# Optimization experiments

Hardware: AMD Instinct MI355X
Metric: run time of the kernel (lower is better)

## Reference

```python
import jax, jax.numpy as jnp
import numpy as np

TREE_DEPTH = 6
IN_F, OUT_F = 1024, 1024
BATCH = 2048
N_LEAVES = 2 ** TREE_DEPTH
N_NODES = N_LEAVES - 1


def _tree_routes(depth):
    """Static routing table: for each leaf, the decision-node index visited at
    each depth and whether the leaf takes the sigmoid (1) or 1-sigmoid (0) branch.
    Mirrors the torch traversal: node = 2*node + 1 + bit; bits of leaf id LSB-first."""
    n_leaves = 2 ** depth
    idx = np.zeros((n_leaves, depth), dtype=np.int32)
    pos = np.zeros((n_leaves, depth), dtype=bool)
    for l in range(n_leaves):
        node, index = 0, l
        for d in range(depth):
            idx[l, d] = node
            pos[l, d] = (index % 2 == 0)
            node = node * 2 + 1 + index % 2
            index >>= 1
    return idx, pos

ROUTE_IDX, ROUTE_POS = _tree_routes(TREE_DEPTH)


def setup_inputs() -> dict:
    key = jax.random.key(0)
    kx, kwd, kwl = jax.random.split(key, 3)
    scale = 0.02  # keep sigmoid/softmax logits in a sane range
    x = jax.random.normal(kx, (BATCH, IN_F), dtype=jnp.float32)
    Wd = jax.random.normal(kwd, (N_NODES, IN_F), dtype=jnp.float32) * scale
    bd = jnp.zeros((N_NODES,), dtype=jnp.float32)
    Wl = jax.random.normal(kwl, (N_LEAVES, OUT_F, IN_F), dtype=jnp.float32) * scale
    bl = jnp.zeros((N_LEAVES, OUT_F), dtype=jnp.float32)
    return {"x": x, "Wd": Wd, "bd": bd, "Wl": Wl, "bl": bl}


def reference(x, Wd, bd, Wl, bl):
    # All decision node probabilities in one GEMM: [B, n_nodes]
    dprob = jax.nn.sigmoid(x @ Wd.T + bd)
    # Gather per-leaf path probs [B, L, depth] and take path product -> routing [B, L]
    path = dprob[:, ROUTE_IDX]                      # [B, L, D]
    path = jnp.where(ROUTE_POS, path, 1.0 - path)
    routing = jnp.prod(path, axis=-1)               # [B, L]
    # All leaf experts in one batched GEMM: [B, L, out], softmax over out (torch dim=1)
    leaf_logits = jnp.einsum('bi,loi->blo', x, Wl) + bl
    leaves = jax.nn.softmax(leaf_logits, axis=-1)
    # Routing-weighted sum over leaves
    return jnp.einsum('bl,blo->bo', routing, leaves)
```

## Files before the change

kernel.cpp:

```cpp
#include <hip/hip_runtime.h>
#include <hip/hip_bf16.h>

#define BATCH 2048
#define KD 1024
#define ND 1024
#define NLEAF 64
#define BM 256
#define BN 256
#define BKT 32
#define NKT (KD / BKT)

typedef __attribute__((ext_vector_type(8))) short bf16x8;
typedef __attribute__((ext_vector_type(4))) float f32x4;
typedef __attribute__((ext_vector_type(4))) _Float16 f16x4;

#define WLB_OFF 0ULL
#define XB_OFF  134217728ULL
#define RT_OFF  138412032ULL
#define LG_OFF  138936320ULL

__device__ __forceinline__ unsigned short f2bf(float f) {
  unsigned int u = __float_as_uint(f);
  u += 0x7fffu + ((u >> 16) & 1u);
  return (unsigned short)(u >> 16);
}

__device__ __forceinline__ void gload_lds16(const void* g, void* l) {
  __builtin_amdgcn_global_load_lds(
      (const __attribute__((address_space(1))) unsigned int*)g,
      (__attribute__((address_space(3))) unsigned int*)l, 16, 0, 0);
}

__global__ void __launch_bounds__(256) convert_kernel(
    const float* __restrict__ Wl, const float* __restrict__ x,
    unsigned short* __restrict__ wlb, unsigned short* __restrict__ xb) {
  const long long WL4 = 16777216LL;
  const long long X4  = 524288LL;
  long long i = (long long)blockIdx.x * 256 + threadIdx.x;
  const long long stride = (long long)gridDim.x * 256;
  for (; i < WL4 + X4; i += stride) {
    float4 v;
    if (i < WL4) v = ((const float4*)Wl)[i];
    else         v = ((const float4*)x)[i - WL4];
    ushort4 o;
    o.x = f2bf(v.x); o.y = f2bf(v.y); o.z = f2bf(v.z); o.w = f2bf(v.w);
    if (i < WL4) ((ushort4*)wlb)[i] = o;
    else         ((ushort4*)xb)[i - WL4] = o;
  }
}

__global__ void __launch_bounds__(256) routing_kernel(
    const float* __restrict__ x, const float* __restrict__ Wd,
    const float* __restrict__ bd, float* __restrict__ rt) {
  __shared__ float xs[4][KD];
  __shared__ float sdp[4][64];
  const int tid = threadIdx.x;
  const int b0 = blockIdx.x * 4;
  const float4* xsrc = (const float4*)(x + (size_t)b0 * KD);
  float4* xdst = (float4*)&xs[0][0];
  for (int i = tid; i < KD; i += 256) xdst[i] = xsrc[i];
  __syncthreads();
  const int wv = tid >> 6, ln = tid & 63;
  const int b = b0 + wv;
  if (ln < 63) {
    const float4* wrow = (const float4*)(Wd + (size_t)ln * KD);
    const float4* xr = (const float4*)&xs[wv][0];
    float4 a = {0.f, 0.f, 0.f, 0.f};
    for (int k = 0; k < KD / 4; ++k) {
      float4 w = wrow[k], xv = xr[k];
      a.x += w.x * xv.x; a.y += w.y * xv.y; a.z += w.z * xv.z; a.w += w.w * xv.w;
    }
    float z = a.x + a.y + a.z + a.w + bd[ln];
    sdp[wv][ln] = 1.f / (1.f + __expf(-z));
  }
  __syncthreads();
  float prod = 1.f;
  int node = 0, index = ln;
  for (int d = 0; d < 6; ++d) {
    float pv = sdp[wv][node];
    prod *= (index & 1) ? (1.f - pv) : pv;
    node = node * 2 + 1 + (index & 1);
    index >>= 1;
  }
  rt[(size_t)b * NLEAF + ln] = prod;
}

__global__ void __launch_bounds__(512, 2) gemm_kernel(
    const unsigned short* __restrict__ A, const unsigned short* __restrict__ B,
    _Float16* __restrict__ C, int ntile) {
  extern __shared__ char smem[];
  const int tid = threadIdx.x;
  const int w = tid >> 6, ln = tid & 63;
  const int wm = w >> 2, wn = w & 3;
  const int g = ln >> 4, r16 = ln & 15;
  const int bid = blockIdx.x;
  const int j = bid >> 3;
  const int bm = (j & 7) * BM;
  const int bn = (((j >> 3) << 3) + (bid & 7)) * BN;
  const long long ldc = (long long)ntile * 256;

  const int rS = tid >> 2;
  const int cS = tid & 3;
  const int csrc = cS ^ ((rS >> 1) & 3);
  const unsigned short* ga0 = A + (size_t)(bm + rS) * KD + csrc * 8;
  const unsigned short* ga1 = ga0 + (size_t)128 * KD;
  const unsigned short* gb0 = B + (size_t)(bn + rS) * KD + csrc * 8;
  const unsigned short* gb1 = gb0 + (size_t)128 * KD;
  const int ldsw = w * 1024;

  auto STAGE_A = [&](int tile) {
    char* base = smem + (tile & 3) * 32768;
    const size_t ko = (size_t)tile * BKT;
    gload_lds16(ga0 + ko, base + ldsw);
    gload_lds16(ga1 + ko, base + 8192 + ldsw);
  };
  auto STAGE_B = [&](int tile) {
    char* base = smem + (tile & 3) * 32768;
    const size_t ko = (size_t)tile * BKT;
    gload_lds16(gb0 + ko, base + 16384 + ldsw);
    gload_lds16(gb1 + ko, base + 24576 + ldsw);
  };

  int offA[8], offB[4];
#pragma unroll
  for (int mi = 0; mi < 8; ++mi) {
    const int row = wm * 128 + mi * 16 + r16;
    offA[mi] = row * 64 + (g ^ ((row >> 1) & 3)) * 16;
  }
#pragma unroll
  for (int ni = 0; ni < 4; ++ni) {
    const int row = wn * 64 + ni * 16 + r16;
    offB[ni] = 16384 + row * 64 + (g ^ ((row >> 1) & 3)) * 16;
  }

  f32x4 acc[8][4];
#pragma unroll
  for (int mi = 0; mi < 8; ++mi)
#pragma unroll
    for (int ni = 0; ni < 4; ++ni) acc[mi][ni] = (f32x4){0.f, 0.f, 0.f, 0.f};

  STAGE_A(0); STAGE_B(0);
  STAGE_A(1); STAGE_B(1);
  STAGE_A(2); STAGE_B(2);
  asm volatile("s_waitcnt vmcnt(8)" ::: "memory");
  asm volatile("s_barrier" ::: "memory");

  for (int t = 0; t < NKT; ++t) {
    const char* buf = smem + (t & 3) * 32768;
    bf16x8 af[4], bfr[4];
#pragma unroll
    for (int ni = 0; ni < 4; ++ni) bfr[ni] = *(const bf16x8*)(buf + offB[ni]);
#pragma unroll
    for (int mi = 0; mi < 4; ++mi) af[mi] = *(const bf16x8*)(buf + offA[mi]);
    if (t + 3 < NKT) STAGE_A(t + 3);
    asm volatile("s_barrier" ::: "memory");
    asm volatile("s_waitcnt lgkmcnt(0)" ::: "memory");
    __builtin_amdgcn_sched_barrier(0);
    __builtin_amdgcn_s_setprio(1);
#pragma unroll
    for (int mi = 0; mi < 4; ++mi)
#pragma unroll
      for (int ni = 0; ni < 4; ++ni)
        acc[mi][ni] = __builtin_amdgcn_mfma_f32_16x16x32_bf16(
            af[mi], bfr[ni], acc[mi][ni], 0, 0, 0);
    __builtin_amdgcn_s_setprio(0);
    __builtin_amdgcn_sched_barrier(0);
#pragma unroll
    for (int mi = 0; mi < 4; ++mi) af[mi] = *(const bf16x8*)(buf + offA[mi + 4]);
    if (t + 3 < NKT) STAGE_B(t + 3);
    asm volatile("s_barrier" ::: "memory");
    asm volatile("s_waitcnt lgkmcnt(0)" ::: "memory");
    __builtin_amdgcn_sched_barrier(0);
    __builtin_amdgcn_s_setprio(1);
#pragma unroll
    for (int mi = 0; mi < 4; ++mi)
#pragma unroll
      for (int ni = 0; ni < 4; ++ni)
        acc[mi + 4][ni] = __builtin_amdgcn_mfma_f32_16x16x32_bf16(
            af[mi], bfr[ni], acc[mi + 4][ni], 0, 0, 0);
    __builtin_amdgcn_s_setprio(0);
    __builtin_amdgcn_sched_barrier(0);
    if (t + 3 < NKT) {
      asm volatile("s_waitcnt vmcnt(8)" ::: "memory");
    } else if (t + 2 < NKT) {
      asm volatile("s_waitcnt vmcnt(4)" ::: "memory");
    } else if (t + 1 < NKT) {
      asm volatile("s_waitcnt vmcnt(0)" ::: "memory");
    }
    if (t + 1 < NKT) asm volatile("s_barrier" ::: "memory");
  }

#pragma unroll
  for (int mi = 0; mi < 8; ++mi)
#pragma unroll
    for (int q = 0; q < 4; ++q) {
      const long long grow = bm + wm * 128 + mi * 16 + g * 4 + q;
#pragma unroll
      for (int ni = 0; ni < 4; ++ni) {
        const int gcol = bn + wn * 64 + ni * 16 + r16;
        C[grow * ldc + gcol] = (_Float16)acc[mi][ni][q];
      }
    }
}

__global__ void __launch_bounds__(256) smax_kernel(
    const _Float16* __restrict__ Cg, const float* __restrict__ rt,
    const float* __restrict__ bl, float* __restrict__ out,
    int lpg, int l0, int first) {
  __shared__ float reds[2][2][4];
  __shared__ float rts[64];
  const int tid = threadIdx.x;
  const int b = blockIdx.x;
  const int w = tid >> 6, ln = tid & 63;
  const int c0 = tid * 4;
  if (tid < lpg) rts[tid] = rt[(size_t)b * NLEAF + l0 + tid];
  __syncthreads();
  float oacc[4] = {0.f, 0.f, 0.f, 0.f};
  const long long ldc = (long long)lpg * ND;

  for (int jj = 0; jj < lpg; jj += 2) {
    const int par = (jj >> 1) & 1;
    const f16x4 h0 = *(const f16x4*)(Cg + (size_t)b * ldc + jj * ND + c0);
    const f16x4 h1 = *(const f16x4*)(Cg + (size_t)b * ldc + (jj + 1) * ND + c0);
    const float4 bv0 = *(const float4*)(bl + (size_t)(l0 + jj) * ND + c0);
    const float4 bv1 = *(const float4*)(bl + (size_t)(l0 + jj + 1) * ND + c0);
    float e0[4], e1[4], s0 = 0.f, s1 = 0.f;
    e0[0] = __expf((float)h0[0] + bv0.x); e0[1] = __expf((float)h0[1] + bv0.y);
    e0[2] = __expf((float)h0[2] + bv0.z); e0[3] = __expf((float)h0[3] + bv0.w);
    e1[0] = __expf((float)h1[0] + bv1.x); e1[1] = __expf((float)h1[1] + bv1.y);
    e1[2] = __expf((float)h1[2] + bv1.z); e1[3] = __expf((float)h1[3] + bv1.w);
#pragma unroll
    for (int k = 0; k < 4; ++k) { s0 += e0[k]; s1 += e1[k]; }
#pragma unroll
    for (int off = 1; off < 64; off <<= 1) {
      s0 += __shfl_xor(s0, off);
      s1 += __shfl_xor(s1, off);
    }
    if (ln == 0) { reds[par][0][w] = s0; reds[par][1][w] = s1; }
    __syncthreads();
    const float S0 = reds[par][0][0] + reds[par][0][1] + reds[par][0][2] + reds[par][0][3];
    const float S1 = reds[par][1][0] + reds[par][1][1] + reds[par][1][2] + reds[par][1][3];
    const float c0f = rts[jj] / S0;
    const float c1f = rts[jj + 1] / S1;
#pragma unroll
    for (int k = 0; k < 4; ++k) oacc[k] += c0f * e0[k] + c1f * e1[k];
  }

  float* orow = out + (size_t)b * ND + c0;
  if (first) {
    *(float4*)orow = (float4){oacc[0], oacc[1], oacc[2], oacc[3]};
  } else {
    float4 p = *(const float4*)orow;
    p.x += oacc[0]; p.y += oacc[1]; p.z += oacc[2]; p.w += oacc[3];
    *(float4*)orow = p;
  }
}

extern "C" void kernel_launch(void* const* d_in, const int* in_sizes, int n_in,
                              void* d_out, int out_size, void* d_ws, size_t ws_size,
                              hipStream_t stream) {
  const float* x  = (const float*)d_in[0];
  const float* Wd = (const float*)d_in[1];
  const float* bd = (const float*)d_in[2];
  const float* Wl = (const float*)d_in[3];
  const float* bl = (const float*)d_in[4];
  float* out = (float*)d_out;
  char* ws = (char*)d_ws;
  unsigned short* wlb = (unsigned short*)(ws + WLB_OFF);
  unsigned short* xb  = (unsigned short*)(ws + XB_OFF);
  float* rt           = (float*)(ws + RT_OFF);
  _Float16* lg        = (_Float16*)(ws + LG_OFF);

  convert_kernel<<<2048, 256, 0, stream>>>(Wl, x, wlb, xb);
  routing_kernel<<<BATCH / 4, 256, 0, stream>>>(x, Wd, bd, rt);
  hipFuncSetAttribute((const void*)gemm_kernel,
                      hipFuncAttributeMaxDynamicSharedMemorySize, 131072);

  const int ngrp = (ws_size >= LG_OFF + (size_t)BATCH * NLEAF * ND * 2) ? 1 : 4;
  const int lpg = NLEAF / ngrp;
  const int ntile = lpg * (ND / BN);
  for (int grp = 0; grp < ngrp; ++grp) {
    gemm_kernel<<<8 * ntile, 512, 131072, stream>>>(
        xb, wlb + (size_t)grp * lpg * ND * KD, lg, ntile);
    smax_kernel<<<BATCH, 256, 0, stream>>>(lg, rt, bl, out,
                                           lpg, grp * lpg, grp == 0);
  }
}
```

Baseline: 507.3 us.

## Switch GEMM mainloop to BK=64 double-buffered tiles with split-half staging

The leaf GEMM mainloop moves from a 4-stage ring of BK=32 tiles to a 2-stage double buffer of BK=64 tiles. Each tile is split into four 16KB regions (A and B, each in two K-halves), and these are prefetched one region at a time between MFMA phases. The aim is to halve the loop iteration count and the per-tile wait/barrier overhead. The cost is extra s_barriers per iteration and a shallower prefetch distance of one tile, which may expose more global-load latency.

```diff
diff --git a/kernel.cpp b/kernel.cpp
--- a/kernel.cpp
+++ b/kernel.cpp
@@ -7,8 +7,8 @@
 #define NLEAF 64
 #define BM 256
 #define BN 256
-#define BKT 32
-#define NKT (KD / BKT)
+#define BKT 64
+#define NT (KD / BKT)
 
 typedef __attribute__((ext_vector_type(8))) short bf16x8;
 typedef __attribute__((ext_vector_type(4))) float f32x4;
@@ -108,29 +108,25 @@
   const unsigned short* gb1 = gb0 + (size_t)128 * KD;
   const int ldsw = w * 1024;
 
-  auto STAGE_A = [&](int tile) {
-    char* base = smem + (tile & 3) * 32768;
-    const size_t ko = (size_t)tile * BKT;
-    gload_lds16(ga0 + ko, base + ldsw);
-    gload_lds16(ga1 + ko, base + 8192 + ldsw);
-  };
-  auto STAGE_B = [&](int tile) {
-    char* base = smem + (tile & 3) * 32768;
-    const size_t ko = (size_t)tile * BKT;
-    gload_lds16(gb0 + ko, base + 16384 + ldsw);
-    gload_lds16(gb1 + ko, base + 24576 + ldsw);
+  auto STAGE_H = [&](int tile, int region) {
+    char* base = smem + (tile & 1) * 65536 + region * 16384;
+    const unsigned short* g0 = (region >= 2) ? gb0 : ga0;
+    const unsigned short* g1 = (region >= 2) ? gb1 : ga1;
+    const size_t ko = (size_t)tile * BKT + (region & 1) * 32;
+    gload_lds16(g0 + ko, base + ldsw);
+    gload_lds16(g1 + ko, base + 8192 + ldsw);
   };
 
   int offA[8], offB[4];
 #pragma unroll
   for (int mi = 0; mi < 8; ++mi) {
     const int row = wm * 128 + mi * 16 + r16;
-    offA[mi] = row * 64 + (g ^ ((row >> 1) & 3)) * 16;
+    offA[mi] = row * 64 + ((g ^ ((row >> 1) & 3)) * 16);
   }
 #pragma unroll
   for (int ni = 0; ni < 4; ++ni) {
     const int row = wn * 64 + ni * 16 + r16;
-    offB[ni] = 16384 + row * 64 + (g ^ ((row >> 1) & 3)) * 16;
+    offB[ni] = row * 64 + ((g ^ ((row >> 1) & 3)) * 16);
   }
 
   f32x4 acc[8][4];
@@ -139,20 +135,22 @@
 #pragma unroll
     for (int ni = 0; ni < 4; ++ni) acc[mi][ni] = (f32x4){0.f, 0.f, 0.f, 0.f};
 
-  STAGE_A(0); STAGE_B(0);
-  STAGE_A(1); STAGE_B(1);
-  STAGE_A(2); STAGE_B(2);
-  asm volatile("s_waitcnt vmcnt(8)" ::: "memory");
+  STAGE_H(0, 0); STAGE_H(0, 2); STAGE_H(0, 1); STAGE_H(0, 3);
+  asm volatile("s_waitcnt vmcnt(4)" ::: "memory");
   asm volatile("s_barrier" ::: "memory");
 
-  for (int t = 0; t < NKT; ++t) {
-    const char* buf = smem + (t & 3) * 32768;
+  for (int t = 0; t < NT; ++t) {
+    const bool pf = (t + 1 < NT);
+    const char* bufp = smem + (t & 1) * 65536;
     bf16x8 af[4], bfr[4];
-#pragma unroll
-    for (int ni = 0; ni < 4; ++ni) bfr[ni] = *(const bf16x8*)(buf + offB[ni]);
-#pragma unroll
-    for (int mi = 0; mi < 4; ++mi) af[mi] = *(const bf16x8*)(buf + offA[mi]);
-    if (t + 3 < NKT) STAGE_A(t + 3);
+
+#pragma unroll
+    for (int ni = 0; ni < 4; ++ni)
+      bfr[ni] = *(const bf16x8*)(bufp + 32768 + offB[ni]);
+#pragma unroll
+    for (int mi = 0; mi < 4; ++mi)
+      af[mi] = *(const bf16x8*)(bufp + offA[mi]);
+    if (pf) STAGE_H(t + 1, 0);
     asm volatile("s_barrier" ::: "memory");
     asm volatile("s_waitcnt lgkmcnt(0)" ::: "memory");
     __builtin_amdgcn_sched_barrier(0);
@@ -165,9 +163,12 @@
             af[mi], bfr[ni], acc[mi][ni], 0, 0, 0);
     __builtin_amdgcn_s_setprio(0);
     __builtin_amdgcn_sched_barrier(0);
-#pragma unroll
-    for (int mi = 0; mi < 4; ++mi) af[mi] = *(const bf16x8*)(buf + offA[mi + 4]);
-    if (t + 3 < NKT) STAGE_B(t + 3);
+    asm volatile("s_barrier" ::: "memory");
+
+#pragma unroll
+    for (int mi = 0; mi < 4; ++mi)
+      af[mi] = *(const bf16x8*)(bufp + offA[mi + 4]);
+    if (pf) STAGE_H(t + 1, 2);
     asm volatile("s_barrier" ::: "memory");
     asm volatile("s_waitcnt lgkmcnt(0)" ::: "memory");
     __builtin_amdgcn_sched_barrier(0);
@@ -180,14 +181,51 @@
             af[mi], bfr[ni], acc[mi + 4][ni], 0, 0, 0);
     __builtin_amdgcn_s_setprio(0);
     __builtin_amdgcn_sched_barrier(0);
-    if (t + 3 < NKT) {
-      asm volatile("s_waitcnt vmcnt(8)" ::: "memory");
-    } else if (t + 2 < NKT) {
+    if (pf) asm volatile("s_waitcnt vmcnt(4)" ::: "memory");
+    else    asm volatile("s_waitcnt vmcnt(0)" ::: "memory");
+    asm volatile("s_barrier" ::: "memory");
+
+#pragma unroll
+    for (int ni = 0; ni < 4; ++ni)
+      bfr[ni] = *(const bf16x8*)(bufp + 49152 + offB[ni]);
+#pragma unroll
+    for (int mi = 0; mi < 4; ++mi)
+      af[mi] = *(const bf16x8*)(bufp + 16384 + offA[mi]);
+    if (pf) STAGE_H(t + 1, 1);
+    asm volatile("s_barrier" ::: "memory");
+    asm volatile("s_waitcnt lgkmcnt(0)" ::: "memory");
+    __builtin_amdgcn_sched_barrier(0);
+    __builtin_amdgcn_s_setprio(1);
+#pragma unroll
+    for (int mi = 0; mi < 4; ++mi)
+#pragma unroll
+      for (int ni = 0; ni < 4; ++ni)
+        acc[mi][ni] = __builtin_amdgcn_mfma_f32_16x16x32_bf16(
+            af[mi], bfr[ni], acc[mi][ni], 0, 0, 0);
+    __builtin_amdgcn_s_setprio(0);
+    __builtin_amdgcn_sched_barrier(0);
+    asm volatile("s_barrier" ::: "memory");
+
+#pragma unroll
+    for (int mi = 0; mi < 4; ++mi)
+      af[mi] = *(const bf16x8*)(bufp + 16384 + offA[mi + 4]);
+    if (pf) STAGE_H(t + 1, 3);
+    asm volatile("s_barrier" ::: "memory");
+    asm volatile("s_waitcnt lgkmcnt(0)" ::: "memory");
+    __builtin_amdgcn_sched_barrier(0);
+    __builtin_amdgcn_s_setprio(1);
+#pragma unroll
+    for (int mi = 0; mi < 4; ++mi)
+#pragma unroll
+      for (int ni = 0; ni < 4; ++ni)
+        acc[mi + 4][ni] = __builtin_amdgcn_mfma_f32_16x16x32_bf16(
+            af[mi], bfr[ni], acc[mi + 4][ni], 0, 0, 0);
+    __builtin_amdgcn_s_setprio(0);
+    __builtin_amdgcn_sched_barrier(0);
+    if (pf) {
       asm volatile("s_waitcnt vmcnt(4)" ::: "memory");
-    } else if (t + 1 < NKT) {
-      asm volatile("s_waitcnt vmcnt(0)" ::: "memory");
+      asm volatile("s_barrier" ::: "memory");
     }
-    if (t + 1 < NKT) asm volatile("s_barrier" ::: "memory");
   }
 
 #pragma unroll
```

Result: no change. 499.8 us (-1.5%).

## Pre-pack x into MFMA fragment layout and load A operand directly to registers

Applied to the files above, without the earlier changes.

The convert kernel now writes the bf16 copy of x in a fragment-packed layout, so each lane of the GEMM can load its A operand straight from global memory into registers, skipping LDS. Only B is staged through LDS, which halves shared memory per block to 64 KB, and A fragments are double-buffered in registers across k-steps with a simpler one-barrier-per-step pipeline. This removes LDS traffic and barriers for A. In exchange it increases register pressure and sends A reads through global memory and cache on every k-step.

```diff
diff --git a/kernel.cpp b/kernel.cpp
--- a/kernel.cpp
+++ b/kernel.cpp
@@ -7,15 +7,13 @@
 #define NLEAF 64
 #define BM 256
 #define BN 256
-#define BKT 32
-#define NKT (KD / BKT)
 
 typedef __attribute__((ext_vector_type(8))) short bf16x8;
 typedef __attribute__((ext_vector_type(4))) float f32x4;
 typedef __attribute__((ext_vector_type(4))) _Float16 f16x4;
 
 #define WLB_OFF 0ULL
-#define XB_OFF  134217728ULL
+#define XP_OFF  134217728ULL
 #define RT_OFF  138412032ULL
 #define LG_OFF  138936320ULL
 
@@ -33,19 +31,28 @@
 
 __global__ void __launch_bounds__(256) convert_kernel(
     const float* __restrict__ Wl, const float* __restrict__ x,
-    unsigned short* __restrict__ wlb, unsigned short* __restrict__ xb) {
+    unsigned short* __restrict__ wlb, unsigned short* __restrict__ xp) {
   const long long WL4 = 16777216LL;
-  const long long X4  = 524288LL;
+  const long long XJ  = 524288LL;
   long long i = (long long)blockIdx.x * 256 + threadIdx.x;
   const long long stride = (long long)gridDim.x * 256;
-  for (; i < WL4 + X4; i += stride) {
-    float4 v;
-    if (i < WL4) v = ((const float4*)Wl)[i];
-    else         v = ((const float4*)x)[i - WL4];
-    ushort4 o;
-    o.x = f2bf(v.x); o.y = f2bf(v.y); o.z = f2bf(v.z); o.w = f2bf(v.w);
-    if (i < WL4) ((ushort4*)wlb)[i] = o;
-    else         ((ushort4*)xb)[i - WL4] = o;
+  for (; i < WL4 + XJ; i += stride) {
+    if (i < WL4) {
+      float4 v = ((const float4*)Wl)[i];
+      ushort4 o;
+      o.x = f2bf(v.x); o.y = f2bf(v.y); o.z = f2bf(v.z); o.w = f2bf(v.w);
+      ((ushort4*)wlb)[i] = o;
+    } else {
+      const long long jj = i - WL4;
+      const int pt = (int)(jj >> 1), half = (int)(jj & 1);
+      const int f = pt >> 6, l = pt & 63;
+      const int row = (f & 127) * 16 + (l & 15);
+      const int k0 = (f >> 7) * 32 + (l >> 4) * 8 + half * 4;
+      float4 v = *(const float4*)(x + (size_t)row * KD + k0);
+      ushort4 o;
+      o.x = f2bf(v.x); o.y = f2bf(v.y); o.z = f2bf(v.z); o.w = f2bf(v.w);
+      *(ushort4*)(xp + (size_t)f * 512 + l * 8 + half * 4) = o;
+    }
   }
 }
 
@@ -85,8 +92,34 @@
   rt[(size_t)b * NLEAF + ln] = prod;
 }
 
+#define GBODY(CUR, NXT, S, VMASM, LAST)                                     \
+  {                                                                          \
+    if (!(LAST)) {                                                           \
+      _Pragma("unroll")                                                      \
+      for (int mi = 0; mi < 8; ++mi)                                         \
+        NXT[mi] = *(const bf16x8*)(apL +                                     \
+            ((size_t)((S) + 1) * 128 + rf0 + mi) * 512);                     \
+    }                                                                        \
+    if ((S) + 2 < 32) STAGE_B((S) + 2);                                      \
+    asm volatile(VMASM ::: "memory");                                        \
+    asm volatile("s_barrier" ::: "memory");                                  \
+    const char* bbuf = smem + ((S) & 3) * 16384;                             \
+    bf16x8 bfr[4];                                                           \
+    _Pragma("unroll")                                                        \
+    for (int ni = 0; ni < 4; ++ni)                                           \
+      bfr[ni] = *(const bf16x8*)(bbuf + offB[ni]);                           \
+    __builtin_amdgcn_s_setprio(1);                                           \
+    _Pragma("unroll")                                                        \
+    for (int mi = 0; mi < 8; ++mi)                                           \
+      _Pragma("unroll")                                                      \
+      for (int ni = 0; ni < 4; ++ni)                                         \
+        acc[mi][ni] = __builtin_amdgcn_mfma_f32_16x16x32_bf16(               \
+            CUR[mi], bfr[ni], acc[mi][ni], 0, 0, 0);                         \
+    __builtin_amdgcn_s_setprio(0);                                           \
+  }
+
 __global__ void __launch_bounds__(512, 2) gemm_kernel(
-    const unsigned short* __restrict__ A, const unsigned short* __restrict__ B,
+    const unsigned short* __restrict__ Ap, const unsigned short* __restrict__ B,
     _Float16* __restrict__ C, int ntile) {
   extern __shared__ char smem[];
   const int tid = threadIdx.x;
@@ -102,36 +135,26 @@
   const int rS = tid >> 2;
   const int cS = tid & 3;
   const int csrc = cS ^ ((rS >> 1) & 3);
-  const unsigned short* ga0 = A + (size_t)(bm + rS) * KD + csrc * 8;
-  const unsigned short* ga1 = ga0 + (size_t)128 * KD;
   const unsigned short* gb0 = B + (size_t)(bn + rS) * KD + csrc * 8;
   const unsigned short* gb1 = gb0 + (size_t)128 * KD;
   const int ldsw = w * 1024;
 
-  auto STAGE_A = [&](int tile) {
-    char* base = smem + (tile & 3) * 32768;
-    const size_t ko = (size_t)tile * BKT;
-    gload_lds16(ga0 + ko, base + ldsw);
-    gload_lds16(ga1 + ko, base + 8192 + ldsw);
+  auto STAGE_B = [&](int s) {
+    char* base = smem + (s & 3) * 16384;
+    const size_t ko = (size_t)s * 32;
+    gload_lds16(gb0 + ko, base + ldsw);
+    gload_lds16(gb1 + ko, base + 8192 + ldsw);
   };
-  auto STAGE_B = [&](int tile) {
-    char* base = smem + (tile & 3) * 32768;
-    const size_t ko = (size_t)tile * BKT;
-    gload_lds16(gb0 + ko, base + 16384 + ldsw);
-    gload_lds16(gb1 + ko, base + 24576 + ldsw);
-  };
-
-  int offA[8], offB[4];
-#pragma unroll
-  for (int mi = 0; mi < 8; ++mi) {
-    const int row = wm * 128 + mi * 16 + r16;
-    offA[mi] = row * 64 + (g ^ ((row >> 1) & 3)) * 16;
-  }
+
+  int offB[4];
 #pragma unroll
   for (int ni = 0; ni < 4; ++ni) {
     const int row = wn * 64 + ni * 16 + r16;
-    offB[ni] = 16384 + row * 64 + (g ^ ((row >> 1) & 3)) * 16;
-  }
+    offB[ni] = row * 64 + (g ^ ((row >> 1) & 3)) * 16;
+  }
+
+  const int rf0 = (bm >> 4) + wm * 8;
+  const unsigned short* apL = Ap + (size_t)ln * 8;
 
   f32x4 acc[8][4];
 #pragma unroll
@@ -139,56 +162,19 @@
 #pragma unroll
     for (int ni = 0; ni < 4; ++ni) acc[mi][ni] = (f32x4){0.f, 0.f, 0.f, 0.f};
 
-  STAGE_A(0); STAGE_B(0);
-  STAGE_A(1); STAGE_B(1);
-  STAGE_A(2); STAGE_B(2);
-  asm volatile("s_waitcnt vmcnt(8)" ::: "memory");
-  asm volatile("s_barrier" ::: "memory");
-
-  for (int t = 0; t < NKT; ++t) {
-    const char* buf = smem + (t & 3) * 32768;
-    bf16x8 af[4], bfr[4];
-#pragma unroll
-    for (int ni = 0; ni < 4; ++ni) bfr[ni] = *(const bf16x8*)(buf + offB[ni]);
-#pragma unroll
-    for (int mi = 0; mi < 4; ++mi) af[mi] = *(const bf16x8*)(buf + offA[mi]);
-    if (t + 3 < NKT) STAGE_A(t + 3);
-    asm volatile("s_barrier" ::: "memory");
-    asm volatile("s_waitcnt lgkmcnt(0)" ::: "memory");
-    __builtin_amdgcn_sched_barrier(0);
-    __builtin_amdgcn_s_setprio(1);
-#pragma unroll
-    for (int mi = 0; mi < 4; ++mi)
-#pragma unroll
-      for (int ni = 0; ni < 4; ++ni)
-        acc[mi][ni] = __builtin_amdgcn_mfma_f32_16x16x32_bf16(
-            af[mi], bfr[ni], acc[mi][ni], 0, 0, 0);
-    __builtin_amdgcn_s_setprio(0);
-    __builtin_amdgcn_sched_barrier(0);
-#pragma unroll
-    for (int mi = 0; mi < 4; ++mi) af[mi] = *(const bf16x8*)(buf + offA[mi + 4]);
-    if (t + 3 < NKT) STAGE_B(t + 3);
-    asm volatile("s_barrier" ::: "memory");
-    asm volatile("s_waitcnt lgkmcnt(0)" ::: "memory");
-    __builtin_amdgcn_sched_barrier(0);
-    __builtin_amdgcn_s_setprio(1);
-#pragma unroll
-    for (int mi = 0; mi < 4; ++mi)
-#pragma unroll
-      for (int ni = 0; ni < 4; ++ni)
-        acc[mi + 4][ni] = __builtin_amdgcn_mfma_f32_16x16x32_bf16(
-            af[mi], bfr[ni], acc[mi + 4][ni], 0, 0, 0);
-    __builtin_amdgcn_s_setprio(0);
-    __builtin_amdgcn_sched_barrier(0);
-    if (t + 3 < NKT) {
-      asm volatile("s_waitcnt vmcnt(8)" ::: "memory");
-    } else if (t + 2 < NKT) {
-      asm volatile("s_waitcnt vmcnt(4)" ::: "memory");
-    } else if (t + 1 < NKT) {
-      asm volatile("s_waitcnt vmcnt(0)" ::: "memory");
-    }
-    if (t + 1 < NKT) asm volatile("s_barrier" ::: "memory");
-  }
+  bf16x8 aE[8], aO[8];
+  STAGE_B(0);
+#pragma unroll
+  for (int mi = 0; mi < 8; ++mi)
+    aE[mi] = *(const bf16x8*)(apL + ((size_t)rf0 + mi) * 512);
+  STAGE_B(1);
+
+  for (int u = 0; u < 15; ++u) {
+    GBODY(aE, aO, 2 * u,     "s_waitcnt vmcnt(10)", false);
+    GBODY(aO, aE, 2 * u + 1, "s_waitcnt vmcnt(10)", false);
+  }
+  GBODY(aE, aO, 30, "s_waitcnt vmcnt(8)", false);
+  GBODY(aO, aE, 31, "s_waitcnt vmcnt(0)", true);
 
 #pragma unroll
   for (int mi = 0; mi < 8; ++mi)
@@ -267,21 +253,21 @@
   float* out = (float*)d_out;
   char* ws = (char*)d_ws;
   unsigned short* wlb = (unsigned short*)(ws + WLB_OFF);
-  unsigned short* xb  = (unsigned short*)(ws + XB_OFF);
+  unsigned short* xp  = (unsigned short*)(ws + XP_OFF);
   float* rt           = (float*)(ws + RT_OFF);
   _Float16* lg        = (_Float16*)(ws + LG_OFF);
 
-  convert_kernel<<<2048, 256, 0, stream>>>(Wl, x, wlb, xb);
+  convert_kernel<<<2048, 256, 0, stream>>>(Wl, x, wlb, xp);
   routing_kernel<<<BATCH / 4, 256, 0, stream>>>(x, Wd, bd, rt);
   hipFuncSetAttribute((const void*)gemm_kernel,
-                      hipFuncAttributeMaxDynamicSharedMemorySize, 131072);
+                      hipFuncAttributeMaxDynamicSharedMemorySize, 65536);
 
   const int ngrp = (ws_size >= LG_OFF + (size_t)BATCH * NLEAF * ND * 2) ? 1 : 4;
   const int lpg = NLEAF / ngrp;
   const int ntile = lpg * (ND / BN);
   for (int grp = 0; grp < ngrp; ++grp) {
-    gemm_kernel<<<8 * ntile, 512, 131072, stream>>>(
-        xb, wlb + (size_t)grp * lpg * ND * KD, lg, ntile);
+    gemm_kernel<<<8 * ntile, 512, 65536, stream>>>(
+        xp, wlb + (size_t)grp * lpg * ND * KD, lg, ntile);
     smax_kernel<<<BATCH, 256, 0, stream>>>(lg, rt, bl, out,
                                            lpg, grp * lpg, grp == 0);
   }
```

Measured after the change: 554.0 us. +9.2%, slower.

## Double-buffer LDS fragments in registers to overlap reads with MFMA

Applied to the files above, without the earlier changes.

Restructures the GEMM main loop so each iteration issues the full 32 MFMAs on register fragments loaded in the previous step, while the LDS reads for the next k-tile are issued ahead. A and B global-to-LDS staging for a tile is merged into one call, and the two half-iteration barriers become one per tile. The aim is to hide LDS read latency and cut barrier count. The cost is twice the fragment registers, which could pressure occupancy under the 512x2 launch bounds.

```diff
diff --git a/kernel.cpp b/kernel.cpp
--- a/kernel.cpp
+++ b/kernel.cpp
@@ -7,8 +7,6 @@
 #define NLEAF 64
 #define BM 256
 #define BN 256
-#define BKT 32
-#define NKT (KD / BKT)
 
 typedef __attribute__((ext_vector_type(8))) short bf16x8;
 typedef __attribute__((ext_vector_type(4))) float f32x4;
@@ -85,6 +83,33 @@
   rt[(size_t)b * NLEAF + ln] = prod;
 }
 
+#define GBODY(CURA, CURB, NXTA, NXTB, S, VMASM, DOREAD)                      \
+  {                                                                          \
+    if ((S) + 3 < 32) STAGE((S) + 3);                                        \
+    asm volatile(VMASM ::: "memory");                                        \
+    asm volatile("s_waitcnt lgkmcnt(0)" ::: "memory");                       \
+    asm volatile("s_barrier" ::: "memory");                                  \
+    if (DOREAD) {                                                            \
+      const char* nbuf = smem + (((S) + 1) & 3) * 32768;                     \
+      _Pragma("unroll")                                                      \
+      for (int mi = 0; mi < 8; ++mi)                                         \
+        NXTA[mi] = *(const bf16x8*)(nbuf + offA[mi]);                        \
+      _Pragma("unroll")                                                      \
+      for (int ni = 0; ni < 4; ++ni)                                         \
+        NXTB[ni] = *(const bf16x8*)(nbuf + 16384 + offB[ni]);                \
+    }                                                                        \
+    __builtin_amdgcn_sched_barrier(0);                                       \
+    __builtin_amdgcn_s_setprio(1);                                           \
+    _Pragma("unroll")                                                        \
+    for (int mi = 0; mi < 8; ++mi)                                           \
+      _Pragma("unroll")                                                      \
+      for (int ni = 0; ni < 4; ++ni)                                         \
+        acc[mi][ni] = __builtin_amdgcn_mfma_f32_16x16x32_bf16(               \
+            CURA[mi], CURB[ni], acc[mi][ni], 0, 0, 0);                       \
+    __builtin_amdgcn_s_setprio(0);                                           \
+    __builtin_amdgcn_sched_barrier(0);                                       \
+  }
+
 __global__ void __launch_bounds__(512, 2) gemm_kernel(
     const unsigned short* __restrict__ A, const unsigned short* __restrict__ B,
     _Float16* __restrict__ C, int ntile) {
@@ -108,15 +133,11 @@
   const unsigned short* gb1 = gb0 + (size_t)128 * KD;
   const int ldsw = w * 1024;
 
-  auto STAGE_A = [&](int tile) {
-    char* base = smem + (tile & 3) * 32768;
-    const size_t ko = (size_t)tile * BKT;
+  auto STAGE = [&](int t) {
+    char* base = smem + (t & 3) * 32768;
+    const size_t ko = (size_t)t * 32;
     gload_lds16(ga0 + ko, base + ldsw);
     gload_lds16(ga1 + ko, base + 8192 + ldsw);
-  };
-  auto STAGE_B = [&](int tile) {
-    char* base = smem + (tile & 3) * 32768;
-    const size_t ko = (size_t)tile * BKT;
     gload_lds16(gb0 + ko, base + 16384 + ldsw);
     gload_lds16(gb1 + ko, base + 24576 + ldsw);
   };
@@ -130,7 +151,7 @@
 #pragma unroll
   for (int ni = 0; ni < 4; ++ni) {
     const int row = wn * 64 + ni * 16 + r16;
-    offB[ni] = 16384 + row * 64 + (g ^ ((row >> 1) & 3)) * 16;
+    offB[ni] = row * 64 + (g ^ ((row >> 1) & 3)) * 16;
   }
 
   f32x4 acc[8][4];
@@ -139,56 +160,27 @@
 #pragma unroll
     for (int ni = 0; ni < 4; ++ni) acc[mi][ni] = (f32x4){0.f, 0.f, 0.f, 0.f};
 
-  STAGE_A(0); STAGE_B(0);
-  STAGE_A(1); STAGE_B(1);
-  STAGE_A(2); STAGE_B(2);
+  bf16x8 aE[8], bE[4], aO[8], bO[4];
+
+  STAGE(0); STAGE(1); STAGE(2);
   asm volatile("s_waitcnt vmcnt(8)" ::: "memory");
   asm volatile("s_barrier" ::: "memory");
-
-  for (int t = 0; t < NKT; ++t) {
-    const char* buf = smem + (t & 3) * 32768;
-    bf16x8 af[4], bfr[4];
-#pragma unroll
-    for (int ni = 0; ni < 4; ++ni) bfr[ni] = *(const bf16x8*)(buf + offB[ni]);
-#pragma unroll
-    for (int mi = 0; mi < 4; ++mi) af[mi] = *(const bf16x8*)(buf + offA[mi]);
-    if (t + 3 < NKT) STAGE_A(t + 3);
-    asm volatile("s_barrier" ::: "memory");
-    asm volatile("s_waitcnt lgkmcnt(0)" ::: "memory");
-    __builtin_amdgcn_sched_barrier(0);
-    __builtin_amdgcn_s_setprio(1);
-#pragma unroll
-    for (int mi = 0; mi < 4; ++mi)
-#pragma unroll
-      for (int ni = 0; ni < 4; ++ni)
-        acc[mi][ni] = __builtin_amdgcn_mfma_f32_16x16x32_bf16(
-            af[mi], bfr[ni], acc[mi][ni], 0, 0, 0);
-    __builtin_amdgcn_s_setprio(0);
-    __builtin_amdgcn_sched_barrier(0);
-#pragma unroll
-    for (int mi = 0; mi < 4; ++mi) af[mi] = *(const bf16x8*)(buf + offA[mi + 4]);
-    if (t + 3 < NKT) STAGE_B(t + 3);
-    asm volatile("s_barrier" ::: "memory");
-    asm volatile("s_waitcnt lgkmcnt(0)" ::: "memory");
-    __builtin_amdgcn_sched_barrier(0);
-    __builtin_amdgcn_s_setprio(1);
-#pragma unroll
-    for (int mi = 0; mi < 4; ++mi)
-#pragma unroll
-      for (int ni = 0; ni < 4; ++ni)
-        acc[mi + 4][ni] = __builtin_amdgcn_mfma_f32_16x16x32_bf16(
-            af[mi], bfr[ni], acc[mi + 4][ni], 0, 0, 0);
-    __builtin_amdgcn_s_setprio(0);
-    __builtin_amdgcn_sched_barrier(0);
-    if (t + 3 < NKT) {
-      asm volatile("s_waitcnt vmcnt(8)" ::: "memory");
-    } else if (t + 2 < NKT) {
-      asm volatile("s_waitcnt vmcnt(4)" ::: "memory");
-    } else if (t + 1 < NKT) {
-      asm volatile("s_waitcnt vmcnt(0)" ::: "memory");
-    }
-    if (t + 1 < NKT) asm volatile("s_barrier" ::: "memory");
-  }
+  {
+    const char* nbuf = smem;
+#pragma unroll
+    for (int mi = 0; mi < 8; ++mi) aE[mi] = *(const bf16x8*)(nbuf + offA[mi]);
+#pragma unroll
+    for (int ni = 0; ni < 4; ++ni) bE[ni] = *(const bf16x8*)(nbuf + 16384 + offB[ni]);
+  }
+
+  for (int u = 0; u < 14; ++u) {
+    GBODY(aE, bE, aO, bO, 2 * u,     "s_waitcnt vmcnt(8)", 1);
+    GBODY(aO, bO, aE, bE, 2 * u + 1, "s_waitcnt vmcnt(8)", 1);
+  }
+  GBODY(aE, bE, aO, bO, 28, "s_waitcnt vmcnt(8)", 1);
+  GBODY(aO, bO, aE, bE, 29, "s_waitcnt vmcnt(4)", 1);
+  GBODY(aE, bE, aO, bO, 30, "s_waitcnt vmcnt(0)", 1);
+  GBODY(aO, bO, aE, bE, 31, "s_waitcnt vmcnt(0)", 0);
 
 #pragma unroll
   for (int mi = 0; mi < 8; ++mi)
```

Result: no change. 501.6 us (-1.1%).
